# Optimization experiments

Measured on AMD Instinct MI355X. Metric: run time of the kernel, lower is better.

Reference implementation:

```python
import jax, jax.numpy as jnp
import numpy as np

N = 50000   # num nodes
E = 800000  # num edges (avg degree 16)
L = 4       # num_blocks
H = 128     # hidden_dim
CD = 3      # coords_dim
VD = 3      # vel_dim
FD = 16     # node feature dim = node_dim - coords_dim - vel_dim
ED = 16     # edge_dim
DIN = 2 * H + ED + 1  # edge MLP input dim = 273


def setup_inputs() -> dict:
    key = jax.random.key(0)
    ks = jax.random.split(key, 32)
    s = 0.05
    inp = {}
    inp['nodes'] = jax.random.normal(ks[0], (N, CD + VD + FD), jnp.float32)
    # avoid self-loops (start==end) so the coord-diff norm is never exactly 0
    start = jax.random.randint(ks[1], (E,), 0, N)
    off = jax.random.randint(ks[2], (E,), 1, N)
    inp['edge_indices'] = jnp.stack([start, (start + off) % N]).astype(jnp.int64)
    inp['edge_features'] = jax.random.normal(ks[3], (E, ED), jnp.float32)
    # node embedding
    inp['emb_w'] = (jax.random.normal(ks[4], (FD, H)) * s).astype(jnp.float32)
    inp['emb_b'] = jnp.zeros((H,), jnp.float32)
    # per-block params, stacked over L blocks
    def w(k, shape):
        return (jax.random.normal(k, shape) * s).astype(jnp.float32)
    inp['ew1'] = w(ks[5], (L, DIN, H)); inp['eb1'] = jnp.zeros((L, H), jnp.float32)
    inp['ew2'] = w(ks[6], (L, H, H));   inp['eb2'] = jnp.zeros((L, H), jnp.float32)
    inp['cw1'] = w(ks[7], (L, H, H));   inp['cb1'] = jnp.zeros((L, H), jnp.float32)
    inp['cw2'] = w(ks[8], (L, H, CD));  inp['cb2'] = jnp.zeros((L, CD), jnp.float32)
    inp['vw1'] = w(ks[9], (L, H, H));   inp['vb1'] = jnp.zeros((L, H), jnp.float32)
    inp['vw2'] = w(ks[10], (L, H, 1));  inp['vb2'] = jnp.zeros((L, 1), jnp.float32)
    inp['nw1'] = w(ks[11], (L, 2 * H, H)); inp['nb1'] = jnp.zeros((L, H), jnp.float32)
    inp['nw2'] = w(ks[12], (L, H, H));  inp['nb2'] = jnp.zeros((L, H), jnp.float32)
    return inp


def _forward(nodes, edge_features, emb_w, emb_b, ew1, eb1, ew2, eb2,
             cw1, cb1, cw2, cb2, vw1, vb1, vw2, vb2, nw1, nb1, nw2, nb2,
             edge_indices):
    silu = jax.nn.silu
    coords = nodes[:, :CD]
    vels = nodes[:, CD:CD + VD]
    h = nodes[:, CD + VD:] @ emb_w + emb_b  # [N, H]
    start, end = edge_indices[0], edge_indices[1]
    n = coords.shape[0]
    # per-node edge counts for the coordinate mean-aggregation
    cnt = jax.ops.segment_sum(jnp.ones((start.shape[0], 1), coords.dtype),
                              start, num_segments=n)
    cnt = jnp.maximum(cnt, 1.0)
    for l in range(L):
        cd = coords[start] - coords[end]                       # [E, CD]
        nrm = jnp.sqrt(jnp.sum(cd * cd, axis=1, keepdims=True))  # [E, 1]
        x = jnp.concatenate([h[start], h[end], nrm, edge_features], axis=1)
        m = silu(silu(x @ ew1[l] + eb1[l]) @ ew2[l] + eb2[l])  # [E, H]
        # coordinate update: mean-aggregated weighted diffs + velocity term
        ct = cd * (silu(m @ cw1[l] + cb1[l]) @ cw2[l] + cb2[l])
        coords = coords + jax.ops.segment_sum(ct, start, num_segments=n) / cnt
        coords = coords + (silu(h @ vw1[l] + vb1[l]) @ vw2[l] + vb2[l]) * vels
        # node update: sum-aggregated messages
        agg = jax.ops.segment_sum(m, start, num_segments=n)    # [N, H]
        h = h + silu(jnp.concatenate([h, agg], axis=1) @ nw1[l] + nb1[l]) @ nw2[l] + nb2[l]
    return coords  # prediction_type == 'coords'


def reference(nodes, edge_indices, edge_features, emb_w, emb_b,
              ew1, eb1, ew2, eb2, cw1, cb1, cw2, cb2,
              vw1, vb1, vw2, vb2, nw1, nb1, nw2, nb2):
    return _forward(nodes, edge_features, emb_w, emb_b, ew1, eb1, ew2, eb2,
                    cw1, cb1, cw2, cb2, vw1, vb1, vw2, vb2,
                    nw1, nb1, nw2, nb2, edge_indices)
```

## Files before the change

kernel.cpp:

```cpp
#include <hip/hip_runtime.h>

constexpr int NN = 50000;
constexpr int EE = 800000;
constexpr int HH = 128;

typedef __attribute__((ext_vector_type(8))) __bf16 bfv8;
typedef __attribute__((ext_vector_type(4))) float f32x4;
typedef unsigned short u16;

__device__ __forceinline__ u16 f2bf(float x){
  unsigned u = __builtin_bit_cast(unsigned, x);
  u = u + 0x7fffu + ((u >> 16) & 1u);
  return (u16)(u >> 16);
}
__device__ __forceinline__ float fsilu(float x){
  return x * __builtin_amdgcn_rcpf(1.f + __expf(-x));
}

template<int KSTEPS, int CB, int RB>
__device__ __forceinline__ void mm_tile(const u16* A, int Rbase, const u16* __restrict__ Bp,
                                        const float* __restrict__ bias, int NB, f32x4* acc){
  const int lane = threadIdx.x & 63;
  #pragma unroll
  for (int cb = 0; cb < CB; ++cb){
    int col = cb*16 + (lane & 15);
    float b = (col < NB) ? bias[col] : 0.f;
    acc[cb] = (f32x4){b, b, b, b};
  }
  const int arow = Rbase + (lane & 15);
  const char* abase = (const char*)A + arow * RB;
  const int kb = (lane >> 4) * 16;
  const int swz = (arow & 7) << 4;
  const bfv8* __restrict__ bq = (const bfv8*)Bp + lane;
  for (int ks = 0; ks < KSTEPS; ++ks){
    bfv8 a = *(const bfv8*)(abase + ((ks*64 + kb) ^ swz));
    #pragma unroll
    for (int cb = 0; cb < CB; ++cb){
      bfv8 b = bq[(ks*CB + cb) * 64];
      acc[cb] = __builtin_amdgcn_mfma_f32_16x16x32_bf16(a, b, acc[cb], 0, 0, 0);
    }
  }
}

template<int CB>
__device__ __forceinline__ void silu_store(const f32x4* acc, u16* dst, int Rbase){
  const int lane = threadIdx.x & 63;
  #pragma unroll
  for (int cb = 0; cb < CB; ++cb){
    #pragma unroll
    for (int j = 0; j < 4; ++j){
      int row = Rbase + ((lane >> 4) << 2) + j;
      int col = cb*16 + (lane & 15);
      float s = fsilu(acc[cb][j]);
      *(u16*)((char*)dst + row*256 + ((col*2) ^ ((row & 7) << 4))) = f2bf(s);
    }
  }
}

struct PackDesc { const float* src; u16* dst; int K; int Nc; int CB; int ksteps; int remap; };
struct PackArgs { PackDesc d[32]; };

__global__ __launch_bounds__(256) void pack_kernel(PackArgs pa){
  PackDesc d = pa.d[blockIdx.x];
  int total = d.ksteps * d.CB * 512;
  for (int p = threadIdx.x; p < total; p += 256){
    int j = p & 7, lane = (p >> 3) & 63, cbk = p >> 9;
    int cb = cbk % d.CB, ks = cbk / d.CB;
    int k = ks*32 + ((lane >> 4) * 8) + j;
    int col = cb*16 + (lane & 15);
    int kk = k;
    if (d.remap && k >= 256) kk = (k < 272) ? (k + 1) : ((k == 272) ? 256 : 0x7fffffff);
    float v = (kk < d.K && col < d.Nc) ? d.src[(size_t)kk * d.Nc + col] : 0.f;
    d.dst[p] = f2bf(v);
  }
}

__global__ __launch_bounds__(256) void embed_kernel(const float* __restrict__ nodes,
    const float* __restrict__ emb_w, const float* __restrict__ emb_b,
    float* __restrict__ hf, u16* __restrict__ hbf, float* __restrict__ coords){
  int t = blockIdx.x * 256 + threadIdx.x;
  int g = t >> 2, q = t & 3;
  if (g >= NN) return;
  const float* x = nodes + (size_t)g * 22;
  float acc[32];
  #pragma unroll
  for (int c = 0; c < 32; ++c) acc[c] = emb_b[q*32 + c];
  for (int k = 0; k < 16; ++k){
    float f = x[6 + k];
    const float* wr = emb_w + k*128 + q*32;
    #pragma unroll
    for (int c = 0; c < 32; ++c) acc[c] += f * wr[c];
  }
  size_t off = (size_t)g * HH + q*32;
  #pragma unroll
  for (int c = 0; c < 32; ++c){ hf[off + c] = acc[c]; hbf[off + c] = f2bf(acc[c]); }
  if (q == 0){
    coords[g*3+0] = x[0]; coords[g*3+1] = x[1]; coords[g*3+2] = x[2];
  }
}

__global__ __launch_bounds__(256) void count_kernel(const int* __restrict__ esrc, int* __restrict__ cnt_i){
  int e = blockIdx.x * 256 + threadIdx.x;
  if (e < EE) atomicAdd(&cnt_i[esrc[e]], 1);
}

__global__ __launch_bounds__(256) void scan_kernel(const int* __restrict__ cnt_i,
    int* __restrict__ row_start, int* __restrict__ fill){
  __shared__ int part[256];
  int t = threadIdx.x;
  int lo = t * 196, hi = lo + 196;
  if (lo > NN) lo = NN;
  if (hi > NN) hi = NN;
  int s = 0;
  for (int i = lo; i < hi; ++i) s += cnt_i[i];
  part[t] = s; __syncthreads();
  for (int d = 1; d < 256; d <<= 1){
    int v = (t >= d) ? part[t-d] : 0;
    __syncthreads();
    part[t] += v;
    __syncthreads();
  }
  int run = part[t] - s;
  for (int i = lo; i < hi; ++i){ row_start[i] = run; fill[i] = run; run += cnt_i[i]; }
  if (t == 255) row_start[NN] = run;
}

__global__ __launch_bounds__(256) void scatter_kernel(const int* __restrict__ esrc,
    const int* __restrict__ edst, int* __restrict__ fill,
    int2* __restrict__ sd_sorted, int* __restrict__ eid_sorted){
  int e = blockIdx.x * 256 + threadIdx.x;
  if (e < EE){
    int s = esrc[e];
    int pos = atomicAdd(&fill[s], 1);
    sd_sorted[pos] = make_int2(s, edst[e]);
    eid_sorted[pos] = e;
  }
}

__global__ __launch_bounds__(256) void edge_kernel(
    const float* __restrict__ coords, const u16* __restrict__ hbf, const float* __restrict__ ef,
    const int2* __restrict__ sd_sorted, const int* __restrict__ eid_sorted,
    const u16* __restrict__ ew1p, const u16* __restrict__ ew2p,
    const u16* __restrict__ cw1p, const u16* __restrict__ cw2p,
    const float* __restrict__ eb1, const float* __restrict__ eb2,
    const float* __restrict__ cb1, const float* __restrict__ cb2,
    float* __restrict__ agg, float* __restrict__ acc_ct){
  __shared__ u16 sX[64 * 320];
  __shared__ float4 s_cdn[64];
  __shared__ int s_src[64];
  __shared__ int s_dst[64];
  __shared__ int s_eid[64];

  const int tid = threadIdx.x, wid = tid >> 6, lane = tid & 63;
  const int R = wid * 16;
  const int e0 = blockIdx.x * 64;

  if (lane < 16){
    int row = R + lane;
    int e = e0 + row;
    int2 sd = sd_sorted[e];
    float cx = coords[sd.x*3+0] - coords[sd.y*3+0];
    float cy = coords[sd.x*3+1] - coords[sd.y*3+1];
    float cz = coords[sd.x*3+2] - coords[sd.y*3+2];
    float nrm = sqrtf(cx*cx + cy*cy + cz*cz);
    s_cdn[row] = make_float4(cx, cy, cz, nrm);
    s_src[row] = sd.x; s_dst[row] = sd.y; s_eid[row] = eid_sorted[e];
  }
  {
    int row = R + (lane >> 2), q = lane & 3;
    int s = s_src[row], d = s_dst[row], eid = s_eid[row];
    const uint4* hs = (const uint4*)(hbf + (size_t)s * HH);
    const uint4* hd = (const uint4*)(hbf + (size_t)d * HH);
    char* xrow = (char*)sX + row*640;
    const int swz = (row & 7) << 4;
    #pragma unroll
    for (int c = 0; c < 4; ++c){
      int ch = q + c*4;
      uint4 v = hs[ch];
      *(uint4*)(xrow + ((ch*16) ^ swz)) = v;
    }
    #pragma unroll
    for (int c = 0; c < 4; ++c){
      int ch = q + c*4;
      uint4 v = hd[ch];
      *(uint4*)(xrow + ((256 + ch*16) ^ swz)) = v;
    }
    {
      float f[8];
      #pragma unroll
      for (int j = 0; j < 8; ++j) f[j] = 0.f;
      if (q < 2){
        const float* efp = ef + (size_t)eid * 16 + q*8;
        #pragma unroll
        for (int j = 0; j < 8; ++j) f[j] = efp[j];
      } else if (q == 2){
        f[0] = s_cdn[row].w;
      }
      uint4 v;
      v.x = f2bf(f[0]) | ((unsigned)f2bf(f[1]) << 16);
      v.y = f2bf(f[2]) | ((unsigned)f2bf(f[3]) << 16);
      v.z = f2bf(f[4]) | ((unsigned)f2bf(f[5]) << 16);
      v.w = f2bf(f[6]) | ((unsigned)f2bf(f[7]) << 16);
      *(uint4*)(xrow + ((512 + q*16) ^ swz)) = v;
    }
  }

  u16* wb = sX + R * 320;
  u16* Mb = wb + 2048;

  f32x4 acc[8];
  mm_tile<9, 8, 640>(sX, R, ew1p, eb1, 128, acc);
  silu_store<8>(acc, wb, 0);

  mm_tile<4, 8, 256>(wb, 0, ew2p, eb2, 128, acc);
  {
    const int rb = (lane >> 4) << 2;
    float run[8];
    #pragma unroll
    for (int cb = 0; cb < 8; ++cb) run[cb] = 0.f;
    #pragma unroll
    for (int j = 0; j < 4; ++j){
      int grow = R + rb + j;
      int src = s_src[grow];
      bool flush = (j == 3) || (s_src[grow + 1] != src);
      #pragma unroll
      for (int cb = 0; cb < 8; ++cb){
        int col = cb*16 + (lane & 15);
        float m = fsilu(acc[cb][j]);
        run[cb] += m;
        *(u16*)((char*)Mb + (rb + j)*256 + ((col*2) ^ (((rb + j) & 7) << 4))) = f2bf(m);
      }
      if (flush){
        #pragma unroll
        for (int cb = 0; cb < 8; ++cb){
          int col = cb*16 + (lane & 15);
          atomicAdd(&agg[(size_t)src * HH + col], run[cb]);
          run[cb] = 0.f;
        }
      }
    }
  }

  mm_tile<4, 8, 256>(Mb, 0, cw1p, cb1, 128, acc);
  silu_store<8>(acc, wb, 0);

  f32x4 a4[1];
  mm_tile<4, 1, 256>(wb, 0, cw2p, cb2, 3, a4);
  {
    int col = lane & 15;
    if (col < 3){
      const int rb = (lane >> 4) << 2;
      float run = 0.f;
      #pragma unroll
      for (int j = 0; j < 4; ++j){
        int grow = R + rb + j;
        float4 cdn = s_cdn[grow];
        float cdv = (col == 0) ? cdn.x : ((col == 1) ? cdn.y : cdn.z);
        run += cdv * a4[0][j];
        int src = s_src[grow];
        if (j == 3 || s_src[grow + 1] != src){
          atomicAdd(&acc_ct[(size_t)src * 3 + col], run);
          run = 0.f;
        }
      }
    }
  }
}

__global__ __launch_bounds__(256) void node_kernel(
    float* __restrict__ coords, float* __restrict__ hf, u16* __restrict__ hbf,
    const float* __restrict__ agg, const float* __restrict__ acc_ct, const int* __restrict__ row_start,
    const float* __restrict__ nodes,
    const u16* __restrict__ vw1p, const u16* __restrict__ vw2p,
    const u16* __restrict__ nw1p, const u16* __restrict__ nw2p,
    const float* __restrict__ vb1, const float* __restrict__ vb2,
    const float* __restrict__ nb1, const float* __restrict__ nb2){
  __shared__ u16 sXn[64 * 256];
  __shared__ u16 sV[64 * 128];
  __shared__ float s_vt[64];

  const int tid = threadIdx.x, wid = tid >> 6, lane = tid & 63;
  const int R = wid * 16;
  const int g0 = blockIdx.x * 64;

  {
    int row = R + (lane >> 2), q = lane & 3, g = g0 + row;
    #pragma unroll
    for (int c = 0; c < 8; ++c){
      int col8 = q*64 + c*8;
      uint4 v = {0, 0, 0, 0};
      if (g < NN){
        if (col8 < 128) v = ((const uint4*)(hbf + (size_t)g * HH))[col8 >> 3];
        else {
          const float* ap = agg + (size_t)g * HH + (col8 - 128);
          float4 a0 = *(const float4*)ap;
          float4 a1 = *(const float4*)(ap + 4);
          v.x = f2bf(a0.x) | ((unsigned)f2bf(a0.y) << 16);
          v.y = f2bf(a0.z) | ((unsigned)f2bf(a0.w) << 16);
          v.z = f2bf(a1.x) | ((unsigned)f2bf(a1.y) << 16);
          v.w = f2bf(a1.z) | ((unsigned)f2bf(a1.w) << 16);
        }
      }
      *(uint4*)((char*)sXn + row*512 + ((col8*2) ^ ((row & 7) << 4))) = v;
    }
  }

  f32x4 acc[8];
  mm_tile<4, 8, 512>(sXn, R, vw1p, vb1, 128, acc);
  silu_store<8>(acc, sV, R);
  f32x4 a1[1];
  mm_tile<4, 1, 256>(sV, R, vw2p, vb2, 1, a1);
  if ((lane & 15) == 0){
    #pragma unroll
    for (int j = 0; j < 4; ++j) s_vt[R + ((lane >> 4) << 2) + j] = a1[0][j];
  }
  if (lane < 16){
    int row = R + lane, g = g0 + row;
    if (g < NN){
      float cn = (float)(row_start[g + 1] - row_start[g]);
      if (cn < 1.f) cn = 1.f;
      float vt = s_vt[row];
      #pragma unroll
      for (int c = 0; c < 3; ++c){
        float val = coords[g*3 + c] + acc_ct[g*3 + c] / cn + vt * nodes[(size_t)g*22 + 3 + c];
        coords[g*3 + c] = val;
      }
    }
  }

  mm_tile<8, 8, 512>(sXn, R, nw1p, nb1, 128, acc);
  silu_store<8>(acc, sV, R);
  mm_tile<4, 8, 256>(sV, R, nw2p, nb2, 128, acc);
  {
    #pragma unroll
    for (int cb = 0; cb < 8; ++cb){
      int col = cb*16 + (lane & 15);
      #pragma unroll
      for (int j = 0; j < 4; ++j){
        int row = R + ((lane >> 4) << 2) + j, g = g0 + row;
        if (g < NN){
          size_t off = (size_t)g * HH + col;
          float h = acc[cb][j] + hf[off];
          hf[off] = h;
          hbf[off] = f2bf(h);
        }
      }
    }
  }
}

extern "C" void kernel_launch(void* const* d_in, const int* in_sizes, int n_in,
                              void* d_out, int out_size, void* d_ws, size_t ws_size,
                              hipStream_t stream){
  const float* nodes = (const float*)d_in[0];
  const int*   eidx  = (const int*)d_in[1];
  const float* ef    = (const float*)d_in[2];
  const float* emb_w = (const float*)d_in[3];
  const float* emb_b = (const float*)d_in[4];
  const float* ew1 = (const float*)d_in[5];
  const float* eb1 = (const float*)d_in[6];
  const float* ew2 = (const float*)d_in[7];
  const float* eb2 = (const float*)d_in[8];
  const float* cw1 = (const float*)d_in[9];
  const float* cb1 = (const float*)d_in[10];
  const float* cw2 = (const float*)d_in[11];
  const float* cb2 = (const float*)d_in[12];
  const float* vw1 = (const float*)d_in[13];
  const float* vb1 = (const float*)d_in[14];
  const float* vw2 = (const float*)d_in[15];
  const float* vb2 = (const float*)d_in[16];
  const float* nw1 = (const float*)d_in[17];
  const float* nb1 = (const float*)d_in[18];
  const float* nw2 = (const float*)d_in[19];
  const float* nb2 = (const float*)d_in[20];

  constexpr size_t WS_NEEDED = 78u * 1024u * 1024u;
  if (ws_size < WS_NEEDED) return;

  char* ws = (char*)d_ws;
  size_t off = 0;
  auto alloc = [&](size_t bytes){ void* p = ws + off; off += (bytes + 255) & ~(size_t)255; return p; };
  float* coords   = (float*)alloc((size_t)NN * 3 * 4);
  float* hf       = (float*)alloc((size_t)NN * HH * 4);
  u16*   hbf      = (u16*)  alloc((size_t)NN * HH * 2);
  float* agg      = (float*)alloc((size_t)NN * 131 * 4);
  float* acc_ct   = agg + (size_t)NN * HH;
  int*   cnt_i    = (int*)  alloc((size_t)NN * 4);
  int*   row_start= (int*)  alloc((size_t)(NN + 1) * 4);
  int*   fill     = (int*)  alloc((size_t)NN * 4);
  int2*  sd_sorted= (int2*) alloc((size_t)EE * 8);
  int*   eid_sorted=(int*)  alloc((size_t)EE * 4);

  constexpr int O_EW1 = 0;
  constexpr int O_EW2 = O_EW1 + 9*8*512;
  constexpr int O_CW1 = O_EW2 + 4*8*512;
  constexpr int O_CW2 = O_CW1 + 4*8*512;
  constexpr int O_VW1 = O_CW2 + 4*1*512;
  constexpr int O_VW2 = O_VW1 + 4*8*512;
  constexpr int O_NW1 = O_VW2 + 4*1*512;
  constexpr int O_NW2 = O_NW1 + 8*8*512;
  constexpr int LAYER_PACK = O_NW2 + 4*8*512;
  u16* packs = (u16*)alloc((size_t)LAYER_PACK * 4 * 2);

  PackArgs pa;
  for (int l = 0; l < 4; ++l){
    u16* base = packs + (size_t)l * LAYER_PACK;
    int i = l * 8;
    pa.d[i+0] = { ew1 + (size_t)l*273*128, base + O_EW1, 273, 128, 8, 9, 1 };
    pa.d[i+1] = { ew2 + (size_t)l*128*128, base + O_EW2, 128, 128, 8, 4, 0 };
    pa.d[i+2] = { cw1 + (size_t)l*128*128, base + O_CW1, 128, 128, 8, 4, 0 };
    pa.d[i+3] = { cw2 + (size_t)l*128*3,   base + O_CW2, 128,   3, 1, 4, 0 };
    pa.d[i+4] = { vw1 + (size_t)l*128*128, base + O_VW1, 128, 128, 8, 4, 0 };
    pa.d[i+5] = { vw2 + (size_t)l*128*1,   base + O_VW2, 128,   1, 1, 4, 0 };
    pa.d[i+6] = { nw1 + (size_t)l*256*128, base + O_NW1, 256, 128, 8, 8, 0 };
    pa.d[i+7] = { nw2 + (size_t)l*128*128, base + O_NW2, 128, 128, 8, 4, 0 };
  }

  pack_kernel<<<32, 256, 0, stream>>>(pa);
  embed_kernel<<<(NN*4 + 255)/256, 256, 0, stream>>>(nodes, emb_w, emb_b, hf, hbf, coords);
  hipMemsetAsync(cnt_i, 0, (size_t)NN * 4, stream);
  count_kernel<<<(EE + 255)/256, 256, 0, stream>>>(eidx, cnt_i);
  scan_kernel<<<1, 256, 0, stream>>>(cnt_i, row_start, fill);
  scatter_kernel<<<(EE + 255)/256, 256, 0, stream>>>(eidx, eidx + EE, fill, sd_sorted, eid_sorted);

  for (int l = 0; l < 4; ++l){
    hipMemsetAsync(agg, 0, (size_t)NN * 131 * 4, stream);
    u16* base = packs + (size_t)l * LAYER_PACK;
    edge_kernel<<<EE/64, 256, 0, stream>>>(coords, hbf, ef, sd_sorted, eid_sorted,
        base + O_EW1, base + O_EW2, base + O_CW1, base + O_CW2,
        eb1 + l*128, eb2 + l*128, cb1 + l*128, cb2 + l*3, agg, acc_ct);
    node_kernel<<<(NN + 63)/64, 256, 0, stream>>>(coords, hf, hbf, agg, acc_ct, row_start, nodes,
        base + O_VW1, base + O_VW2, base + O_NW1, base + O_NW2,
        vb1 + l*128, vb2 + l, nb1 + l*128, nb2 + l*128);
  }

  hipMemcpyAsync(d_out, coords, (size_t)NN * 3 * 4, hipMemcpyDeviceToDevice, stream);
}
```

Measured before the change: 2.244 ms.

## Load first-layer MFMA operands directly from global instead of staging in LDS

The edge and node kernels no longer stage the gathered h[src], h[dst], edge features and agg rows into a large shared-memory tile. Each lane now loads its MFMA A-fragment straight from global memory, converting to bf16 in registers. LDS use drops to small per-wave buffers for the intermediate activations, which may allow higher occupancy and removes a store/reload round trip. The trade-off is scattered 16-byte global loads feeding the MFMAs directly, with less latency hiding, and the matmul loops are now fully unrolled.

```diff
diff --git a/kernel.cpp b/kernel.cpp
--- a/kernel.cpp
+++ b/kernel.cpp
@@ -17,9 +17,11 @@
   return x * __builtin_amdgcn_rcpf(1.f + __expf(-x));
 }
 
-template<int KSTEPS, int CB, int RB>
-__device__ __forceinline__ void mm_tile(const u16* A, int Rbase, const u16* __restrict__ Bp,
-                                        const float* __restrict__ bias, int NB, f32x4* acc){
+__device__ __forceinline__ bfv8 mfma_a_from(const f32x4 a){ return __builtin_bit_cast(bfv8, a); }
+
+template<int KSTEPS, int CB>
+__device__ __forceinline__ void mm_lds(const u16* Arows, const u16* __restrict__ Bp,
+                                       const float* __restrict__ bias, int NB, f32x4* acc){
   const int lane = threadIdx.x & 63;
   #pragma unroll
   for (int cb = 0; cb < CB; ++cb){
@@ -27,29 +29,28 @@
     float b = (col < NB) ? bias[col] : 0.f;
     acc[cb] = (f32x4){b, b, b, b};
   }
-  const int arow = Rbase + (lane & 15);
-  const char* abase = (const char*)A + arow * RB;
+  const int arow = lane & 15;
+  const char* abase = (const char*)Arows + arow * 256;
   const int kb = (lane >> 4) * 16;
   const int swz = (arow & 7) << 4;
   const bfv8* __restrict__ bq = (const bfv8*)Bp + lane;
+  #pragma unroll
   for (int ks = 0; ks < KSTEPS; ++ks){
     bfv8 a = *(const bfv8*)(abase + ((ks*64 + kb) ^ swz));
     #pragma unroll
-    for (int cb = 0; cb < CB; ++cb){
-      bfv8 b = bq[(ks*CB + cb) * 64];
-      acc[cb] = __builtin_amdgcn_mfma_f32_16x16x32_bf16(a, b, acc[cb], 0, 0, 0);
-    }
+    for (int cb = 0; cb < CB; ++cb)
+      acc[cb] = __builtin_amdgcn_mfma_f32_16x16x32_bf16(a, bq[(ks*CB + cb) * 64], acc[cb], 0, 0, 0);
   }
 }
 
 template<int CB>
-__device__ __forceinline__ void silu_store(const f32x4* acc, u16* dst, int Rbase){
+__device__ __forceinline__ void silu_store(const f32x4* acc, u16* dst){
   const int lane = threadIdx.x & 63;
   #pragma unroll
   for (int cb = 0; cb < CB; ++cb){
     #pragma unroll
     for (int j = 0; j < 4; ++j){
-      int row = Rbase + ((lane >> 4) << 2) + j;
+      int row = ((lane >> 4) << 2) + j;
       int col = cb*16 + (lane & 15);
       float s = fsilu(acc[cb][j]);
       *(u16*)((char*)dst + row*256 + ((col*2) ^ ((row & 7) << 4))) = f2bf(s);
@@ -145,10 +146,10 @@
     const float* __restrict__ eb1, const float* __restrict__ eb2,
     const float* __restrict__ cb1, const float* __restrict__ cb2,
     float* __restrict__ agg, float* __restrict__ acc_ct){
-  __shared__ u16 sX[64 * 320];
+  __shared__ __align__(16) u16 sM1[4][2048];
+  __shared__ __align__(16) u16 sMb[4][2048];
   __shared__ float4 s_cdn[64];
   __shared__ int s_src[64];
-  __shared__ int s_dst[64];
   __shared__ int s_eid[64];
 
   const int tid = threadIdx.x, wid = tid >> 6, lane = tid & 63;
@@ -164,103 +165,107 @@
     float cz = coords[sd.x*3+2] - coords[sd.y*3+2];
     float nrm = sqrtf(cx*cx + cy*cy + cz*cz);
     s_cdn[row] = make_float4(cx, cy, cz, nrm);
-    s_src[row] = sd.x; s_dst[row] = sd.y; s_eid[row] = eid_sorted[e];
+    s_src[row] = sd.x; s_eid[row] = eid_sorted[e];
   }
   {
-    int row = R + (lane >> 2), q = lane & 3;
-    int s = s_src[row], d = s_dst[row], eid = s_eid[row];
-    const uint4* hs = (const uint4*)(hbf + (size_t)s * HH);
-    const uint4* hd = (const uint4*)(hbf + (size_t)d * HH);
-    char* xrow = (char*)sX + row*640;
-    const int swz = (row & 7) << 4;
-    #pragma unroll
-    for (int c = 0; c < 4; ++c){
-      int ch = q + c*4;
-      uint4 v = hs[ch];
-      *(uint4*)(xrow + ((ch*16) ^ swz)) = v;
-    }
-    #pragma unroll
-    for (int c = 0; c < 4; ++c){
-      int ch = q + c*4;
-      uint4 v = hd[ch];
-      *(uint4*)(xrow + ((256 + ch*16) ^ swz)) = v;
-    }
+    const int myrow = R + (lane & 15);
+    const int g = lane >> 4;
+    int e = e0 + myrow;
+    int2 sd = sd_sorted[e];
+    const u16* hsb = hbf + (size_t)sd.x * HH + g*8;
+    const u16* hdb = hbf + (size_t)sd.y * HH + g*8;
+    const int my_eid = s_eid[myrow];
+
+    f32x4 acc[8];
     {
-      float f[8];
-      #pragma unroll
-      for (int j = 0; j < 8; ++j) f[j] = 0.f;
-      if (q < 2){
-        const float* efp = ef + (size_t)eid * 16 + q*8;
+      const bfv8* __restrict__ bq = (const bfv8*)ew1p + lane;
+      #pragma unroll
+      for (int cb = 0; cb < 8; ++cb){
+        float b = eb1[cb*16 + (lane & 15)];
+        acc[cb] = (f32x4){b, b, b, b};
+      }
+      #pragma unroll
+      for (int ks = 0; ks < 4; ++ks){
+        bfv8 a = *(const bfv8*)(hsb + ks*32);
         #pragma unroll
-        for (int j = 0; j < 8; ++j) f[j] = efp[j];
-      } else if (q == 2){
-        f[0] = s_cdn[row].w;
-      }
-      uint4 v;
-      v.x = f2bf(f[0]) | ((unsigned)f2bf(f[1]) << 16);
-      v.y = f2bf(f[2]) | ((unsigned)f2bf(f[3]) << 16);
-      v.z = f2bf(f[4]) | ((unsigned)f2bf(f[5]) << 16);
-      v.w = f2bf(f[6]) | ((unsigned)f2bf(f[7]) << 16);
-      *(uint4*)(xrow + ((512 + q*16) ^ swz)) = v;
-    }
-  }
-
-  u16* wb = sX + R * 320;
-  u16* Mb = wb + 2048;
-
-  f32x4 acc[8];
-  mm_tile<9, 8, 640>(sX, R, ew1p, eb1, 128, acc);
-  silu_store<8>(acc, wb, 0);
-
-  mm_tile<4, 8, 256>(wb, 0, ew2p, eb2, 128, acc);
-  {
-    const int rb = (lane >> 4) << 2;
-    float run[8];
-    #pragma unroll
-    for (int cb = 0; cb < 8; ++cb) run[cb] = 0.f;
-    #pragma unroll
-    for (int j = 0; j < 4; ++j){
-      int grow = R + rb + j;
-      int src = s_src[grow];
-      bool flush = (j == 3) || (s_src[grow + 1] != src);
-      #pragma unroll
-      for (int cb = 0; cb < 8; ++cb){
-        int col = cb*16 + (lane & 15);
-        float m = fsilu(acc[cb][j]);
-        run[cb] += m;
-        *(u16*)((char*)Mb + (rb + j)*256 + ((col*2) ^ (((rb + j) & 7) << 4))) = f2bf(m);
-      }
-      if (flush){
+        for (int cb = 0; cb < 8; ++cb)
+          acc[cb] = __builtin_amdgcn_mfma_f32_16x16x32_bf16(a, bq[(ks*8 + cb)*64], acc[cb], 0, 0, 0);
+      }
+      #pragma unroll
+      for (int ks = 4; ks < 8; ++ks){
+        bfv8 a = *(const bfv8*)(hdb + (ks - 4)*32);
+        #pragma unroll
+        for (int cb = 0; cb < 8; ++cb)
+          acc[cb] = __builtin_amdgcn_mfma_f32_16x16x32_bf16(a, bq[(ks*8 + cb)*64], acc[cb], 0, 0, 0);
+      }
+      union { bfv8 v; u16 s[8]; unsigned u[4]; } at;
+      at.u[0] = at.u[1] = at.u[2] = at.u[3] = 0u;
+      if (g < 2){
+        float4 f0 = *(const float4*)(ef + (size_t)my_eid * 16 + g*8);
+        float4 f1 = *(const float4*)(ef + (size_t)my_eid * 16 + g*8 + 4);
+        at.u[0] = f2bf(f0.x) | ((unsigned)f2bf(f0.y) << 16);
+        at.u[1] = f2bf(f0.z) | ((unsigned)f2bf(f0.w) << 16);
+        at.u[2] = f2bf(f1.x) | ((unsigned)f2bf(f1.y) << 16);
+        at.u[3] = f2bf(f1.z) | ((unsigned)f2bf(f1.w) << 16);
+      } else if (g == 2){
+        at.s[0] = f2bf(s_cdn[myrow].w);
+      }
+      #pragma unroll
+      for (int cb = 0; cb < 8; ++cb)
+        acc[cb] = __builtin_amdgcn_mfma_f32_16x16x32_bf16(at.v, bq[(8*8 + cb)*64], acc[cb], 0, 0, 0);
+    }
+    silu_store<8>(acc, sM1[wid]);
+
+    mm_lds<4, 8>(sM1[wid], ew2p, eb2, 128, acc);
+    {
+      const int rb = (lane >> 4) << 2;
+      float run[8];
+      #pragma unroll
+      for (int cb = 0; cb < 8; ++cb) run[cb] = 0.f;
+      #pragma unroll
+      for (int j = 0; j < 4; ++j){
+        int lrow = rb + j, grow = R + lrow;
+        int src = s_src[grow];
+        bool flush = (j == 3) || (s_src[grow + 1] != src);
         #pragma unroll
         for (int cb = 0; cb < 8; ++cb){
           int col = cb*16 + (lane & 15);
-          atomicAdd(&agg[(size_t)src * HH + col], run[cb]);
-          run[cb] = 0.f;
+          float m = fsilu(acc[cb][j]);
+          run[cb] += m;
+          *(u16*)((char*)sMb[wid] + lrow*256 + ((col*2) ^ ((lrow & 7) << 4))) = f2bf(m);
         }
-      }
-    }
-  }
-
-  mm_tile<4, 8, 256>(Mb, 0, cw1p, cb1, 128, acc);
-  silu_store<8>(acc, wb, 0);
-
-  f32x4 a4[1];
-  mm_tile<4, 1, 256>(wb, 0, cw2p, cb2, 3, a4);
-  {
-    int col = lane & 15;
-    if (col < 3){
-      const int rb = (lane >> 4) << 2;
-      float run = 0.f;
-      #pragma unroll
-      for (int j = 0; j < 4; ++j){
-        int grow = R + rb + j;
-        float4 cdn = s_cdn[grow];
-        float cdv = (col == 0) ? cdn.x : ((col == 1) ? cdn.y : cdn.z);
-        run += cdv * a4[0][j];
-        int src = s_src[grow];
-        if (j == 3 || s_src[grow + 1] != src){
-          atomicAdd(&acc_ct[(size_t)src * 3 + col], run);
-          run = 0.f;
+        if (flush){
+          #pragma unroll
+          for (int cb = 0; cb < 8; ++cb){
+            int col = cb*16 + (lane & 15);
+            atomicAdd(&agg[(size_t)src * HH + col], run[cb]);
+            run[cb] = 0.f;
+          }
+        }
+      }
+    }
+
+    mm_lds<4, 8>(sMb[wid], cw1p, cb1, 128, acc);
+    silu_store<8>(acc, sM1[wid]);
+
+    f32x4 a4[1];
+    mm_lds<4, 1>(sM1[wid], cw2p, cb2, 3, a4);
+    {
+      int col = lane & 15;
+      if (col < 3){
+        const int rb = (lane >> 4) << 2;
+        float run = 0.f;
+        #pragma unroll
+        for (int j = 0; j < 4; ++j){
+          int grow = R + rb + j;
+          float4 cdn = s_cdn[grow];
+          float cdv = (col == 0) ? cdn.x : ((col == 1) ? cdn.y : cdn.z);
+          run += cdv * a4[0][j];
+          int src = s_src[grow];
+          if (j == 3 || s_src[grow + 1] != src){
+            atomicAdd(&acc_ct[(size_t)src * 3 + col], run);
+            run = 0.f;
+          }
         }
       }
     }
@@ -275,71 +280,96 @@
     const u16* __restrict__ nw1p, const u16* __restrict__ nw2p,
     const float* __restrict__ vb1, const float* __restrict__ vb2,
     const float* __restrict__ nb1, const float* __restrict__ nb2){
-  __shared__ u16 sXn[64 * 256];
-  __shared__ u16 sV[64 * 128];
+  __shared__ __align__(16) u16 sV[4][2048];
   __shared__ float s_vt[64];
 
   const int tid = threadIdx.x, wid = tid >> 6, lane = tid & 63;
   const int R = wid * 16;
   const int g0 = blockIdx.x * 64;
 
+  const int myrow = R + (lane & 15);
+  const int gnode = g0 + myrow;
+  const int arow = (gnode < NN) ? gnode : (NN - 1);
+  const int g = lane >> 4;
+  const u16*  hb = hbf + (size_t)arow * HH + g*8;
+  const float* ab = agg + (size_t)arow * HH + g*8;
+
+  f32x4 acc[8];
   {
-    int row = R + (lane >> 2), q = lane & 3, g = g0 + row;
-    #pragma unroll
-    for (int c = 0; c < 8; ++c){
-      int col8 = q*64 + c*8;
-      uint4 v = {0, 0, 0, 0};
-      if (g < NN){
-        if (col8 < 128) v = ((const uint4*)(hbf + (size_t)g * HH))[col8 >> 3];
-        else {
-          const float* ap = agg + (size_t)g * HH + (col8 - 128);
-          float4 a0 = *(const float4*)ap;
-          float4 a1 = *(const float4*)(ap + 4);
-          v.x = f2bf(a0.x) | ((unsigned)f2bf(a0.y) << 16);
-          v.y = f2bf(a0.z) | ((unsigned)f2bf(a0.w) << 16);
-          v.z = f2bf(a1.x) | ((unsigned)f2bf(a1.y) << 16);
-          v.w = f2bf(a1.z) | ((unsigned)f2bf(a1.w) << 16);
-        }
-      }
-      *(uint4*)((char*)sXn + row*512 + ((col8*2) ^ ((row & 7) << 4))) = v;
-    }
-  }
-
-  f32x4 acc[8];
-  mm_tile<4, 8, 512>(sXn, R, vw1p, vb1, 128, acc);
-  silu_store<8>(acc, sV, R);
+    const bfv8* __restrict__ bq = (const bfv8*)vw1p + lane;
+    #pragma unroll
+    for (int cb = 0; cb < 8; ++cb){
+      float b = vb1[cb*16 + (lane & 15)];
+      acc[cb] = (f32x4){b, b, b, b};
+    }
+    #pragma unroll
+    for (int ks = 0; ks < 4; ++ks){
+      bfv8 a = *(const bfv8*)(hb + ks*32);
+      #pragma unroll
+      for (int cb = 0; cb < 8; ++cb)
+        acc[cb] = __builtin_amdgcn_mfma_f32_16x16x32_bf16(a, bq[(ks*8 + cb)*64], acc[cb], 0, 0, 0);
+    }
+  }
+  silu_store<8>(acc, sV[wid]);
   f32x4 a1[1];
-  mm_tile<4, 1, 256>(sV, R, vw2p, vb2, 1, a1);
+  mm_lds<4, 1>(sV[wid], vw2p, vb2, 1, a1);
   if ((lane & 15) == 0){
     #pragma unroll
     for (int j = 0; j < 4; ++j) s_vt[R + ((lane >> 4) << 2) + j] = a1[0][j];
   }
   if (lane < 16){
-    int row = R + lane, g = g0 + row;
-    if (g < NN){
-      float cn = (float)(row_start[g + 1] - row_start[g]);
+    int row = R + lane, gg = g0 + row;
+    if (gg < NN){
+      float cn = (float)(row_start[gg + 1] - row_start[gg]);
       if (cn < 1.f) cn = 1.f;
       float vt = s_vt[row];
       #pragma unroll
       for (int c = 0; c < 3; ++c){
-        float val = coords[g*3 + c] + acc_ct[g*3 + c] / cn + vt * nodes[(size_t)g*22 + 3 + c];
-        coords[g*3 + c] = val;
-      }
-    }
-  }
-
-  mm_tile<8, 8, 512>(sXn, R, nw1p, nb1, 128, acc);
-  silu_store<8>(acc, sV, R);
-  mm_tile<4, 8, 256>(sV, R, nw2p, nb2, 128, acc);
+        float val = coords[gg*3 + c] + acc_ct[gg*3 + c] / cn + vt * nodes[(size_t)gg*22 + 3 + c];
+        coords[gg*3 + c] = val;
+      }
+    }
+  }
+
+  {
+    const bfv8* __restrict__ bq = (const bfv8*)nw1p + lane;
+    #pragma unroll
+    for (int cb = 0; cb < 8; ++cb){
+      float b = nb1[cb*16 + (lane & 15)];
+      acc[cb] = (f32x4){b, b, b, b};
+    }
+    #pragma unroll
+    for (int ks = 0; ks < 4; ++ks){
+      bfv8 a = *(const bfv8*)(hb + ks*32);
+      #pragma unroll
+      for (int cb = 0; cb < 8; ++cb)
+        acc[cb] = __builtin_amdgcn_mfma_f32_16x16x32_bf16(a, bq[(ks*8 + cb)*64], acc[cb], 0, 0, 0);
+    }
+    #pragma unroll
+    for (int ks = 4; ks < 8; ++ks){
+      float4 f0 = *(const float4*)(ab + (ks - 4)*32);
+      float4 f1 = *(const float4*)(ab + (ks - 4)*32 + 4);
+      union { bfv8 v; unsigned u[4]; } aa;
+      aa.u[0] = f2bf(f0.x) | ((unsigned)f2bf(f0.y) << 16);
+      aa.u[1] = f2bf(f0.z) | ((unsigned)f2bf(f0.w) << 16);
+      aa.u[2] = f2bf(f1.x) | ((unsigned)f2bf(f1.y) << 16);
+      aa.u[3] = f2bf(f1.z) | ((unsigned)f2bf(f1.w) << 16);
+      #pragma unroll
+      for (int cb = 0; cb < 8; ++cb)
+        acc[cb] = __builtin_amdgcn_mfma_f32_16x16x32_bf16(aa.v, bq[(ks*8 + cb)*64], acc[cb], 0, 0, 0);
+    }
+  }
+  silu_store<8>(acc, sV[wid]);
+  mm_lds<4, 8>(sV[wid], nw2p, nb2, 128, acc);
   {
     #pragma unroll
     for (int cb = 0; cb < 8; ++cb){
       int col = cb*16 + (lane & 15);
       #pragma unroll
       for (int j = 0; j < 4; ++j){
-        int row = R + ((lane >> 4) << 2) + j, g = g0 + row;
-        if (g < NN){
-          size_t off = (size_t)g * HH + col;
+        int row = R + ((lane >> 4) << 2) + j, gg = g0 + row;
+        if (gg < NN){
+          size_t off = (size_t)gg * HH + col;
           float h = acc[cb][j] + hf[off];
           hf[off] = h;
           hbf[off] = f2bf(h);
```

Result: slower. 2.374 ms (+5.8%).
